# Optimization experiments

Measured on AMD Instinct MI355X. Metric: run time of the kernel, lower is better.

Reference implementation:

```python
import jax, jax.numpy as jnp
import numpy as np

N_ATOMS = 128
BATCH = 512


def _build_buffers(n):
    # Segments: all non-adjacent bond pairs (i,i+1,j,j+1), j >= i+2, j+1 <= n-1.
    segs = np.array([(i, i + 1, j, j + 1)
                     for i in range(n - 3)
                     for j in range(i + 2, n - 1)], dtype=np.int32)  # (S,4)

    def pidx(a, b):  # linear index of pair (a,b), a<b, in row-major triu(offset=1) order
        return a * n - a * (a + 1) // 2 + (b - a - 1)

    # Each writhe value scatters into its 4 incident residue pairs.
    # Pairs (0,1) [triu idx 0] and (n-2,n-1) [last triu idx] are never incident,
    # so ranks among interior pairs are (triu idx - 1); they are re-inserted by pad.
    inc = []
    for (i, _, j, _) in segs:
        for (a, b) in ((i, j), (i, j + 1), (i + 1, j), (i + 1, j + 1)):
            inc.append(pidx(a, b) - 1)
    indices = np.array(inc, dtype=np.int32)  # (4*S,)

    # Sort permutation placing [upper-triu values, lower-triu values] into
    # row-major order of all off-diagonal (r,c) entries, keyed by r*n + c.
    iu = np.stack(np.triu_indices(n, 1))  # (2, P) row-major
    vals = np.concatenate([iu[0] * n + iu[1], iu[1] * n + iu[0]])
    sort = np.argsort(vals).astype(np.int32)  # (n^2 - n,)
    return segs, indices, sort


def setup_inputs() -> dict:
    key = jax.random.key(0)
    xyz = jax.random.normal(key, (BATCH, N_ATOMS, 3), dtype=jnp.float32)
    segs, indices, sort = _build_buffers(N_ATOMS)
    return {
        "xyz": xyz,
        "segments": jnp.asarray(segs),
        "indices": jnp.asarray(indices),
        "sort": jnp.asarray(sort),
    }


def _divnorm(x):
    return x / jnp.linalg.norm(x, axis=-1, keepdims=True)


def _writhe(xyz, segments):
    # xyz: (B,N,3); segments: (S,4) -> writhe per segment pair, (B,S)
    B, S = xyz.shape[0], segments.shape[0]
    p = xyz[:, segments]  # (B,S,4,3) gathered endpoints [s1a,s1b,s2a,s2b]
    # d[k] = normalize(p_{2+j} - p_i), k = 2*i + j  (the 4 inter-segment directions)
    d = _divnorm((p[:, :, None, 2:, :] - p[:, :, :2, None, :]).reshape(B, S, 4, 3))
    axial = jnp.cross(p[:, :, 3] - p[:, :, 2], p[:, :, 1] - p[:, :, 0])  # (B,S,3)
    signs = jnp.sign(jnp.sum(axial * d[:, :, 0], -1))  # (B,S)
    # 4 face normals of the spherical quadrilateral, then Gauss-Bonnet angle sum
    nrm = _divnorm(jnp.cross(d[:, :, jnp.array([0, 1, 3, 2])],
                             d[:, :, jnp.array([1, 3, 2, 0])]))  # (B,S,4,3)
    cosang = jnp.clip(jnp.sum(nrm * nrm[:, :, jnp.array([1, 2, 3, 0])], -1), -1.0, 1.0)
    omega = jnp.arcsin(cosang).sum(-1)  # (B,S)
    return omega * signs / (2.0 * jnp.pi)


def _laplacian(wr, indices, sort, n):
    # wr: (B,S); scatter-add each writhe into its 4 incident residue pairs,
    # pad back the two untouched pairs, symmetrize, and sort into row-major
    # off-diagonal order -> (B, n^2 - n)
    M = (n * n - n) // 2 - 2
    triu = jnp.zeros((wr.shape[0], M), wr.dtype).at[:, indices].add(
        jnp.repeat(wr, 4, axis=1))
    padded = jnp.pad(triu, ((0, 0), (1, 1)))
    return jnp.concatenate([padded, padded], axis=1)[:, sort]


def reference(xyz, segments, indices, sort):
    xyz = xyz.reshape(-1, N_ATOMS, 3)
    wr = _writhe(xyz, segments)
    return _laplacian(wr, indices, sort, N_ATOMS)
```

## Files before the change

### kernel.cpp

```cpp
#include <hip/hip_runtime.h>
#include <math.h>

#define NATOMS    128
#define NSEG      7875
#define NSEG_PAD  8192
#define NPAIR     8128
#define OUT_PER_B 16256
#define BLOCK     512

typedef float v2f __attribute__((ext_vector_type(2)));
__device__ __forceinline__ v2f mk2(float a, float b) { v2f r; r.x = a; r.y = b; return r; }

struct P3 { v2f x, y, z; };
__device__ __forceinline__ P3 psub(P3 a, P3 b) { return {a.x - b.x, a.y - b.y, a.z - b.z}; }
__device__ __forceinline__ P3 pcross(P3 a, P3 b) {
    return {a.y * b.z - a.z * b.y, a.z * b.x - a.x * b.z, a.x * b.y - a.y * b.x};
}
__device__ __forceinline__ v2f pdot(P3 a, P3 b) { return a.x * b.x + a.y * b.y + a.z * b.z; }
__device__ __forceinline__ v2f prsq(v2f q) {
    v2f r; r.x = __builtin_amdgcn_rsqf(q.x); r.y = __builtin_amdgcn_rsqf(q.y); return r;
}
__device__ __forceinline__ v2f pclip1(v2f x) {
    return __builtin_elementwise_min(__builtin_elementwise_max(x, mk2(-1.f, -1.f)),
                                     mk2(1.f, 1.f));
}

__device__ __forceinline__ v2f fast_asin2(v2f x) {
    v2f a = __builtin_elementwise_abs(x);
    v2f p = mk2(-0.0187293f, -0.0187293f);
    p = p * a + mk2( 0.0742610f,  0.0742610f);
    p = p * a + mk2(-0.2121144f, -0.2121144f);
    p = p * a + mk2( 1.5707288f,  1.5707288f);
    v2f om = mk2(1.0f, 1.0f) - a;
    v2f sq; sq.x = __builtin_amdgcn_sqrtf(om.x); sq.y = __builtin_amdgcn_sqrtf(om.y);
    v2f r = mk2(1.57079632679f, 1.57079632679f) - sq * p;
    return __builtin_elementwise_copysign(r, x);
}

__device__ __forceinline__ int seg_row_base(int i) { return 125 * i - (__umul24(i, i - 1) >> 1); }

__device__ __forceinline__ P3 pack3(const float4 &a, const float4 &b) {
    return { mk2(a.x, b.x), mk2(a.y, b.y), mk2(a.z, b.z) };
}

__device__ __forceinline__ v2f seg_writhe_pair(unsigned pa, unsigned pb,
                                               const float4* sp4) {
    int jA = (int)(pa & 127u), iA = (int)(pa >> 7);
    int jB = (int)(pb & 127u), iB = (int)(pb >> 7);

    float4 A0 = sp4[iA], A1 = sp4[iA + 1], A2 = sp4[jA], A3 = sp4[jA + 1];
    float4 B0 = sp4[iB], B1 = sp4[iB + 1], B2 = sp4[jB], B3 = sp4[jB + 1];

    P3 p0 = pack3(A0, B0);
    P3 p1 = pack3(A1, B1);
    P3 p2 = pack3(A2, B2);
    P3 p3 = pack3(A3, B3);

    P3 u0 = psub(p2, p0);
    P3 u1 = psub(p3, p0);
    P3 u2 = psub(p2, p1);
    P3 u3 = psub(p3, p1);

    P3 n0 = pcross(u0, u1);
    P3 n1 = pcross(u1, u3);
    P3 n2 = pcross(u3, u2);
    P3 n3 = pcross(u2, u0);

    v2f q0 = pdot(n0, n0);
    v2f q1 = pdot(n1, n1);
    v2f q2 = pdot(n2, n2);
    v2f q3 = pdot(n3, n3);

    v2f c0 = pclip1(pdot(n0, n1) * prsq(q0 * q1));
    v2f c1 = pclip1(pdot(n1, n2) * prsq(q1 * q2));
    v2f c2 = pclip1(pdot(n2, n3) * prsq(q2 * q3));
    v2f c3 = pclip1(pdot(n3, n0) * prsq(q3 * q0));

    v2f sd = pdot(n2, u0);
    v2f omega = fast_asin2(c0) + fast_asin2(c1) + fast_asin2(c2) + fast_asin2(c3);

    v2f sgn;
    sgn.x = (sd.x > 0.f) ? -1.f : ((sd.x < 0.f) ? 1.f : 0.f);
    sgn.y = (sd.y > 0.f) ? -1.f : ((sd.y < 0.f) ? 1.f : 0.f);

    return omega * sgn * mk2(0.15915494309189535f, 0.15915494309189535f);
}

__global__ __launch_bounds__(BLOCK, 2) void writhe_fused(
    const float* __restrict__ xyz,
    float*       __restrict__ out)
{
    __shared__ float4 sp4[NATOMS];
    __shared__ float  swr[NSEG_PAD];
    __shared__ unsigned short sidx[NSEG_PAD];

    const int b = blockIdx.x;
    const int t = threadIdx.x;

    if (t < 3 * NATOMS) {
        float v = xyz[(size_t)b * (3 * NATOMS) + t];
        int a = t / 3, c = t - 3 * a;
        ((float*)&sp4[a])[c] = v;
    }

    {
        int s = t * 16;
        if (s < NSEG) {
            int i = (int)((251.0f - __builtin_amdgcn_sqrtf(63001.0f - 8.0f * (float)s)) * 0.5f);
            i = max(i, 0);
            i += (seg_row_base(i + 1) <= s);
            i += (seg_row_base(i + 1) <= s);
            i -= (seg_row_base(i) > s);
            i -= (seg_row_base(i) > s);
            int j = s - seg_row_base(i) + i + 2;
            #pragma unroll
            for (int k = 0; k < 16; ++k) {
                if (s < NSEG) sidx[s] = (unsigned short)((i << 7) | j);
                ++s; ++j;
                if (j > 126) { ++i; j = i + 2; }
            }
        }
        if (t < NSEG_PAD - NSEG) sidx[NSEG + t] = (unsigned short)((124 << 7) | 126);
    }
    __syncthreads();

    #pragma unroll
    for (int g = 0; g < 4; ++g) {
        const int sA = g * 2048 + t;
        v2f w1 = seg_writhe_pair(sidx[sA],        sidx[sA + 512],  sp4);
        v2f w2 = seg_writhe_pair(sidx[sA + 1024], sidx[sA + 1536], sp4);
        swr[sA]        = w1.x;
        swr[sA + 512]  = w1.y;
        swr[sA + 1024] = w2.x;
        swr[sA + 1536] = w2.y;
    }
    __syncthreads();

    float* ob = out + (size_t)b * OUT_PER_B;
    for (int k = t; k < OUT_PER_B; k += BLOCK) {
        const int r = (int)(((unsigned)k * 132105u) >> 24);
        int c = k - r * 127;
        c += (c >= r);
        const int a  = min(r, c);
        const int bb = max(r, c);

        const int am1 = a - 1;
        const int s00 = 125 * am1 - ((am1 * (am1 - 1)) >> 1) + bb - a - 2;
        const int s10 = s00 + 125 - a;

        const bool v00 = (a >= 1) && (a <= 125) && (bb >= a + 2);
        const bool v01 = (a >= 1) && (a <= 125) && (bb <= 126);
        const bool v10 = (a <= 124) && (bb >= a + 3);
        const bool v11 = (a <= 124) && (bb <= 126) && (bb >= a + 2);

        const int c00 = min(max(s00,     0), NSEG - 1);
        const int c01 = min(max(s00 + 1, 0), NSEG - 1);
        const int c10 = min(max(s10,     0), NSEG - 1);
        const int c11 = min(max(s10 + 1, 0), NSEG - 1);

        float sum = (v00 ? swr[c00] : 0.0f) + (v01 ? swr[c01] : 0.0f)
                  + (v10 ? swr[c10] : 0.0f) + (v11 ? swr[c11] : 0.0f);

        __builtin_nontemporal_store(sum, ob + k);
    }
}

extern "C" void kernel_launch(void* const* d_in, const int* in_sizes, int n_in,
                              void* d_out, int out_size, void* d_ws, size_t ws_size,
                              hipStream_t stream) {
    const float* xyz = (const float*)d_in[0];
    float*       out = (float*)d_out;

    int B = in_sizes[0] / (NATOMS * 3);
    writhe_fused<<<B, BLOCK, 0, stream>>>(xyz, out);
}
```

Before: 91.84 us.

## Precompute segment and output gather tables in workspace via separate kernel

Adds a small pre-kernel that builds the segment index table and a per-output table of four packed byte offsets into the shared writhe array, with a zero slot standing in for invalid contributions. The main kernel reads these tables from global memory instead of rebuilding the segment index in shared memory and recomputing index arithmetic and validity masks per output. It also drops the shared sidx array, which lowers LDS use. The cost is an extra launch and global or L2 table reads per block, and the fused kernel remains as a fallback when no workspace is provided.

```diff
diff --git a/kernel.cpp b/kernel.cpp
--- a/kernel.cpp
+++ b/kernel.cpp
@@ -4,9 +4,12 @@
 #define NATOMS    128
 #define NSEG      7875
 #define NSEG_PAD  8192
-#define NPAIR     8128
 #define OUT_PER_B 16256
 #define BLOCK     512
+#define TBLOCK    512
+#define SIDX_BYTES 16384
+#define WS_NEED   (SIDX_BYTES + OUT_PER_B * 8)
+#define ZSLOT_OFF (NSEG_PAD * 4)
 
 typedef float v2f __attribute__((ext_vector_type(2)));
 __device__ __forceinline__ v2f mk2(float a, float b) { v2f r; r.x = a; r.y = b; return r; }
@@ -39,6 +42,16 @@
 
 __device__ __forceinline__ int seg_row_base(int i) { return 125 * i - (__umul24(i, i - 1) >> 1); }
 
+__device__ __forceinline__ void seed_ij(int s, int &i, int &j) {
+    i = (int)((251.0f - __builtin_amdgcn_sqrtf(63001.0f - 8.0f * (float)s)) * 0.5f);
+    i = max(i, 0);
+    i += (seg_row_base(i + 1) <= s);
+    i += (seg_row_base(i + 1) <= s);
+    i -= (seg_row_base(i) > s);
+    i -= (seg_row_base(i) > s);
+    j = s - seg_row_base(i) + i + 2;
+}
+
 __device__ __forceinline__ P3 pack3(const float4 &a, const float4 &b) {
     return { mk2(a.x, b.x), mk2(a.y, b.y), mk2(a.z, b.z) };
 }
@@ -86,33 +99,106 @@
     return omega * sgn * mk2(0.15915494309189535f, 0.15915494309189535f);
 }
 
+__global__ __launch_bounds__(TBLOCK) void build_tables(
+    unsigned short* __restrict__ gseg,
+    uint2*          __restrict__ ptab)
+{
+    const int tid = blockIdx.x * TBLOCK + threadIdx.x;
+
+    if (tid < NSEG_PAD) {
+        int i, j;
+        if (tid < NSEG) { seed_ij(tid, i, j); }
+        else            { i = 124; j = 126; }
+        gseg[tid] = (unsigned short)((i << 7) | j);
+    } else {
+        const int k = tid - NSEG_PAD;
+        if (k < OUT_PER_B) {
+            const int r = (int)(((unsigned)k * 132105u) >> 24);
+            int c = k - r * 127;
+            c += (c >= r);
+            const int a  = min(r, c);
+            const int bb = max(r, c);
+
+            const int am1 = a - 1;
+            const int s00 = 125 * am1 - ((am1 * (am1 - 1)) >> 1) + bb - a - 2;
+            const int s10 = s00 + 125 - a;
+
+            const bool v00 = (a >= 1) && (a <= 125) && (bb >= a + 2);
+            const bool v01 = (a >= 1) && (a <= 125) && (bb <= 126);
+            const bool v10 = (a <= 124) && (bb >= a + 3);
+            const bool v11 = (a <= 124) && (bb <= 126) && (bb >= a + 2);
+
+            const unsigned o00 = v00 ? (unsigned)(s00 << 2)       : (unsigned)ZSLOT_OFF;
+            const unsigned o01 = v01 ? (unsigned)((s00 + 1) << 2) : (unsigned)ZSLOT_OFF;
+            const unsigned o10 = v10 ? (unsigned)(s10 << 2)       : (unsigned)ZSLOT_OFF;
+            const unsigned o11 = v11 ? (unsigned)((s10 + 1) << 2) : (unsigned)ZSLOT_OFF;
+
+            ptab[k] = make_uint2(o00 | (o01 << 16), o10 | (o11 << 16));
+        }
+    }
+}
+
+__global__ __launch_bounds__(BLOCK, 2) void writhe_main(
+    const float*          __restrict__ xyz,
+    const unsigned short* __restrict__ gseg,
+    const uint2*          __restrict__ ptab,
+    float*                __restrict__ out)
+{
+    __shared__ float4 sp4[NATOMS];
+    __shared__ float  swr[NSEG_PAD + 1];
+
+    const int b = blockIdx.x;
+    const int t = threadIdx.x;
+
+    if (t < 3 * NATOMS) {
+        float v = xyz[(size_t)b * (3 * NATOMS) + t];
+        int a = t / 3, c = t - 3 * a;
+        ((float*)&sp4[a])[c] = v;
+    }
+    if (t == 0) swr[NSEG_PAD] = 0.0f;
+    __syncthreads();
+
+    #pragma unroll
+    for (int g = 0; g < 4; ++g) {
+        const int sA = g * 2048 + t;
+        v2f w1 = seg_writhe_pair(gseg[sA],        gseg[sA + 512],  sp4);
+        v2f w2 = seg_writhe_pair(gseg[sA + 1024], gseg[sA + 1536], sp4);
+        swr[sA]        = w1.x;
+        swr[sA + 512]  = w1.y;
+        swr[sA + 1024] = w2.x;
+        swr[sA + 1536] = w2.y;
+    }
+    __syncthreads();
+
+    float* ob = out + (size_t)b * OUT_PER_B;
+    const char* swb = (const char*)swr;
+    for (int k = t; k < OUT_PER_B; k += BLOCK) {
+        const uint2 e = ptab[k];
+        const float s0 = *(const float*)(swb + (e.x & 0xFFFFu));
+        const float s1 = *(const float*)(swb + (e.x >> 16));
+        const float s2 = *(const float*)(swb + (e.y & 0xFFFFu));
+        const float s3 = *(const float*)(swb + (e.y >> 16));
+        __builtin_nontemporal_store(s0 + s1 + s2 + s3, ob + k);
+    }
+}
+
 __global__ __launch_bounds__(BLOCK, 2) void writhe_fused(
-    const float* __restrict__ xyz,
-    float*       __restrict__ out)
+    const float* __restrict__ xyz, float* __restrict__ out)
 {
     __shared__ float4 sp4[NATOMS];
     __shared__ float  swr[NSEG_PAD];
     __shared__ unsigned short sidx[NSEG_PAD];
-
     const int b = blockIdx.x;
     const int t = threadIdx.x;
-
     if (t < 3 * NATOMS) {
         float v = xyz[(size_t)b * (3 * NATOMS) + t];
         int a = t / 3, c = t - 3 * a;
         ((float*)&sp4[a])[c] = v;
     }
-
     {
         int s = t * 16;
         if (s < NSEG) {
-            int i = (int)((251.0f - __builtin_amdgcn_sqrtf(63001.0f - 8.0f * (float)s)) * 0.5f);
-            i = max(i, 0);
-            i += (seg_row_base(i + 1) <= s);
-            i += (seg_row_base(i + 1) <= s);
-            i -= (seg_row_base(i) > s);
-            i -= (seg_row_base(i) > s);
-            int j = s - seg_row_base(i) + i + 2;
+            int i, j; seed_ij(s, i, j);
             #pragma unroll
             for (int k = 0; k < 16; ++k) {
                 if (s < NSEG) sidx[s] = (unsigned short)((i << 7) | j);
@@ -123,7 +209,6 @@
         if (t < NSEG_PAD - NSEG) sidx[NSEG + t] = (unsigned short)((124 << 7) | 126);
     }
     __syncthreads();
-
     #pragma unroll
     for (int g = 0; g < 4; ++g) {
         const int sA = g * 2048 + t;
@@ -135,7 +220,6 @@
         swr[sA + 1536] = w2.y;
     }
     __syncthreads();
-
     float* ob = out + (size_t)b * OUT_PER_B;
     for (int k = t; k < OUT_PER_B; k += BLOCK) {
         const int r = (int)(((unsigned)k * 132105u) >> 24);
@@ -143,24 +227,19 @@
         c += (c >= r);
         const int a  = min(r, c);
         const int bb = max(r, c);
-
         const int am1 = a - 1;
         const int s00 = 125 * am1 - ((am1 * (am1 - 1)) >> 1) + bb - a - 2;
         const int s10 = s00 + 125 - a;
-
         const bool v00 = (a >= 1) && (a <= 125) && (bb >= a + 2);
         const bool v01 = (a >= 1) && (a <= 125) && (bb <= 126);
         const bool v10 = (a <= 124) && (bb >= a + 3);
         const bool v11 = (a <= 124) && (bb <= 126) && (bb >= a + 2);
-
         const int c00 = min(max(s00,     0), NSEG - 1);
         const int c01 = min(max(s00 + 1, 0), NSEG - 1);
         const int c10 = min(max(s10,     0), NSEG - 1);
         const int c11 = min(max(s10 + 1, 0), NSEG - 1);
-
         float sum = (v00 ? swr[c00] : 0.0f) + (v01 ? swr[c01] : 0.0f)
                   + (v10 ? swr[c10] : 0.0f) + (v11 ? swr[c11] : 0.0f);
-
         __builtin_nontemporal_store(sum, ob + k);
     }
 }
@@ -172,5 +251,14 @@
     float*       out = (float*)d_out;
 
     int B = in_sizes[0] / (NATOMS * 3);
-    writhe_fused<<<B, BLOCK, 0, stream>>>(xyz, out);
-}
+
+    if (d_ws != nullptr && ws_size >= (size_t)WS_NEED) {
+        unsigned short* gseg = (unsigned short*)d_ws;
+        uint2*          ptab = (uint2*)((char*)d_ws + SIDX_BYTES);
+        const int tgrid = (NSEG_PAD + OUT_PER_B + TBLOCK - 1) / TBLOCK;
+        build_tables<<<tgrid, TBLOCK, 0, stream>>>(gseg, ptab);
+        writhe_main<<<B, BLOCK, 0, stream>>>(xyz, gseg, ptab, out);
+    } else {
+        writhe_fused<<<B, BLOCK, 0, stream>>>(xyz, out);
+    }
+}
```

Measured after the change: 88.19 us. 4.0% less time.
